# Performance work log

Hardware: AMD Instinct MI355X
Metric: run time of the kernel (lower is better)

Reference implementation:

```python
import jax, jax.numpy as jnp
import numpy as np

B, S, D_IN, M, H, F, L, D_OUT = 4, 1024, 256, 1024, 16, 8, 2, 256
HD = M // H
EPS = 1e-5


def setup_inputs() -> dict:
    key = jax.random.key(0)
    ks = iter(jax.random.split(key, 40))
    w = lambda *s: 0.02 * jax.random.normal(next(ks), s, dtype=jnp.float32)
    inp = {
        "x": jax.random.normal(next(ks), (B, S, D_IN), dtype=jnp.float32),
        # phase embedding params
        "Wemb": w(D_IN, M), "bemb": w(M),
        "Wamp": w(M, F), "bamp": w(F),
        "freqs": jnp.logspace(-1, 2, F, dtype=jnp.float32),
        "phase_off": w(F),
        # per-layer attention params, stacked on leading L axis
        "Wq": w(L, M, M), "bq": w(L, M),
        "Wk": w(L, M, M), "bk": w(L, M),
        "Wv": w(L, M, M), "bv": w(L, M),
        "Wo": w(L, M, M), "bo": w(L, M),
        "pbias": w(L, H, F),
        "ln_g": jnp.ones((L, M), dtype=jnp.float32),
        "ln_b": jnp.zeros((L, M), dtype=jnp.float32),
        # output projection MLP
        "W1": w(M, M // 2), "b1": w(M // 2),
        "W2": w(M // 2, D_OUT), "b2": w(D_OUT),
    }
    return inp


def _forward(x, Wemb, bemb, Wamp, bamp, freqs, phase_off,
             Wq, bq, Wk, bk, Wv, bv, Wo, bo, pbias, ln_g, ln_b,
             W1, b1, W2, b2):
    Bsz, Seq, _ = x.shape
    # --- TemporalPhaseEmbedding ---
    m = x @ Wemb + bemb                                   # [B,S,M]
    tc = jnp.arange(Seq, dtype=x.dtype) / Seq * (2.0 * jnp.pi)  # [S]
    amp = jax.nn.softmax(m @ Wamp + bamp, axis=-1)        # [B,S,F]
    pc = tc[:, None] * freqs[None, :] + phase_off         # [S,F] (batch-identical)
    # |m[...,None] * amp * e^{i*pc}| averaged over F == |m| * mean_F(amp)
    pf = jnp.abs(m) * jnp.mean(amp, axis=-1, keepdims=True)  # [B,S,M]
    # phase-coherence, batch-independent since pc is shared across batch
    coh = jnp.cos(pc[:, None, :] - pc[None, :, :])        # [S,S,F]
    scale = 1.0 / jnp.sqrt(jnp.asarray(HD, dtype=x.dtype))
    for l in range(L):
        res = pf
        Q = (pf @ Wq[l] + bq[l]).reshape(Bsz, Seq, H, HD)
        K = (pf @ Wk[l] + bk[l]).reshape(Bsz, Seq, H, HD)
        V = (pf @ Wv[l] + bv[l]).reshape(Bsz, Seq, H, HD)
        bias = jnp.einsum('stf,hf->hst', coh, pbias[l])   # [H,S,S]
        scores = jnp.einsum('bshd,bthd->bhst', Q, K) * scale + bias[None]
        w_attn = jax.nn.softmax(scores, axis=-1)
        att = jnp.einsum('bhst,bthd->bshd', w_attn, V).reshape(Bsz, Seq, M)
        att = att @ Wo[l] + bo[l]
        y = att + res
        mu = jnp.mean(y, axis=-1, keepdims=True)
        var = jnp.var(y, axis=-1, keepdims=True)
        pf = (y - mu) / jnp.sqrt(var + EPS) * ln_g[l] + ln_b[l]
    hdn = jax.nn.relu(pf @ W1 + b1)
    return hdn @ W2 + b2                                  # [B,S,D_OUT]


def reference(x, Wemb, bemb, Wamp, bamp, freqs, phase_off,
              Wq, bq, Wk, bk, Wv, bv, Wo, bo, pbias, ln_g, ln_b,
              W1, b1, W2, b2):
    return _forward(x, Wemb, bemb, Wamp, bamp, freqs, phase_off,
                    Wq, bq, Wk, bk, Wv, bv, Wo, bo, pbias, ln_g, ln_b,
                    W1, b1, W2, b2)
```

## Files before the change

### kernel.cpp

```cpp
#include <hip/hip_runtime.h>
#include <cmath>

#define B_    4
#define S_    1024
#define DIN_  256
#define M_    1024
#define H_    16
#define F_    8
#define L_    2
#define DOUT_ 256
#define NT_   4096

typedef unsigned short u16;
typedef unsigned int   u32;
typedef __bf16 bf16x8 __attribute__((ext_vector_type(8)));
typedef __bf16 bf16x4v __attribute__((ext_vector_type(4)));
typedef float  f32x4  __attribute__((ext_vector_type(4)));

#define LOG2E 1.4426950408889634f
#define QSCALE (0.125f * LOG2E)

__device__ __forceinline__ u16 f2b(float f) {
    u32 u = __builtin_bit_cast(u32, f);
    u += 0x7fffu + ((u >> 16) & 1u);
    return (u16)(u >> 16);
}
__device__ __forceinline__ float b2f(u32 h) {
    return __builtin_bit_cast(float, h << 16);
}
__device__ __forceinline__ void gload_lds16(const void* g, void* l) {
    __builtin_amdgcn_global_load_lds(
        (const __attribute__((address_space(1))) u32*)g,
        (__attribute__((address_space(3))) u32*)l, 16, 0, 0);
}

__device__ __forceinline__ void tileT(float (*t)[33], const float* src,
                                      u16* dst, int K, int N, int n0, int k0,
                                      int tid)
{
    const int r = tid >> 3, c4 = (tid & 7) << 2;
    float4 v = *(const float4*)(src + (size_t)(k0 + r) * N + n0 + c4);
    t[r][c4 + 0] = v.x; t[r][c4 + 1] = v.y; t[r][c4 + 2] = v.z; t[r][c4 + 3] = v.w;
    __syncthreads();
    ushort4 o = make_ushort4(f2b(t[c4 + 0][r]), f2b(t[c4 + 1][r]),
                             f2b(t[c4 + 2][r]), f2b(t[c4 + 3][r]));
    *(ushort4*)(dst + (size_t)(n0 + r) * K + k0 + c4) = o;
}

__global__ __launch_bounds__(256) void prep_k(
    const float* __restrict__ x, const float* __restrict__ Wemb,
    const float* __restrict__ Wq, const float* __restrict__ Wk,
    const float* __restrict__ Wv, const float* __restrict__ Wo,
    const float* __restrict__ W1, const float* __restrict__ W2,
    const float* __restrict__ freqs, const float* __restrict__ poff,
    const float* __restrict__ pb, const float* __restrict__ bq,
    const float* __restrict__ bk, const float* __restrict__ bv,
    u16* __restrict__ xb, u16* __restrict__ WembT, u16* __restrict__ WqkvT,
    u16* __restrict__ WoT, u16* __restrict__ W1T, u16* __restrict__ W2T,
    u16* __restrict__ qcs, u16* __restrict__ csb, float* __restrict__ bqkv)
{
    __shared__ float t[32][33];
    const int bid = blockIdx.x, tid = threadIdx.x;

    if (bid < 1024) {
        int i = (bid * 256 + tid) * 4;
        float4 v = *(const float4*)(x + i);
        *(ushort4*)(xb + i) = make_ushort4(f2b(v.x), f2b(v.y), f2b(v.z), f2b(v.w));
    } else if (bid < 7168) {
        int id = bid - 1024;
        int z = id >> 10, rem = id & 1023;
        int n0 = (rem & 31) << 5, k0 = (rem >> 5) << 5;
        int l = z / 3, which = z - l * 3;
        const float* src = (which == 0 ? Wq : which == 1 ? Wk : Wv) + (size_t)l * M_ * M_;
        u16* d = WqkvT + (size_t)l * 3072 * 1024 + (size_t)which * 1024 * 1024;
        tileT(t, src, d, 1024, 1024, n0, k0, tid);
    } else if (bid < 9216) {
        int id = bid - 7168;
        int z = id >> 10, rem = id & 1023;
        int n0 = (rem & 31) << 5, k0 = (rem >> 5) << 5;
        tileT(t, Wo + (size_t)z * M_ * M_, WoT + (size_t)z * M_ * M_,
              1024, 1024, n0, k0, tid);
    } else if (bid < 9472) {
        int id = bid - 9216;
        int n0 = (id & 31) << 5, k0 = (id >> 5) << 5;
        tileT(t, Wemb, WembT, 256, 1024, n0, k0, tid);
    } else if (bid < 9984) {
        int id = bid - 9472;
        int n0 = (id & 15) << 5, k0 = (id >> 4) << 5;
        tileT(t, W1, W1T, 1024, 512, n0, k0, tid);
    } else if (bid < 10112) {
        int id = bid - 9984;
        int n0 = (id & 7) << 5, k0 = (id >> 3) << 5;
        tileT(t, W2, W2T, 512, 256, n0, k0, tid);
    } else if (bid < 12224) {
        const int QN = L_ * H_ * S_ * 16;
        int idx = (bid - 10112) * 256 + tid;
        if (idx < QN) {
            int f2 = idx & 15, f = f2 & 7;
            int s = (idx >> 4) & 1023;
            int lh = idx >> 14;
            float pc = ((float)s * (6.283185307179586f / 1024.f)) * freqs[f] + poff[f];
            float v = (f2 < 8) ? cosf(pc) : sinf(pc);
            qcs[idx] = f2b(pb[lh * 8 + f] * v * LOG2E);
        } else {
            int i2 = idx - QN;
            int f2 = i2 & 15, f = f2 & 7;
            int s = i2 >> 4;
            float pc = ((float)s * (6.283185307179586f / 1024.f)) * freqs[f] + poff[f];
            csb[i2] = f2b((f2 < 8) ? cosf(pc) : sinf(pc));
        }
    } else {
        int idx = (bid - 12224) * 256 + tid;
        int l = idx >= 3072;
        int j = idx - l * 3072;
        float v = (j < 1024) ? bq[l * 1024 + j]
                : (j < 2048) ? bk[l * 1024 + j - 1024]
                             : bv[l * 1024 + j - 2048];
        bqkv[idx] = v;
    }
}

template<int EPI, int OUTBF, int BM>
__global__ __launch_bounds__(256, 2) void mgemm_k(
    const u16* __restrict__ A, const u16* __restrict__ Wt,
    const float* __restrict__ bias, void* __restrict__ Cout,
    u16* __restrict__ vt, int N, int K)
{
    constexpr int MR = BM / 32;
    __shared__ __attribute__((aligned(16))) u16 As[BM * 64];
    __shared__ __attribute__((aligned(16))) u16 Bs[128 * 64];
    const int tid = threadIdx.x;
    const int lane = tid & 63;
    const int bn = blockIdx.x, bm = blockIdx.y;
    const int wid = tid >> 6, wr = wid >> 1, wc = wid & 1;

    f32x4 acc[MR][4];
#pragma unroll
    for (int m = 0; m < MR; ++m)
#pragma unroll
        for (int n = 0; n < 4; ++n) {
            f32x4 z = {0.f, 0.f, 0.f, 0.f};
            acc[m][n] = z;
        }

    const int r = lane & 15, g = lane >> 4;
    const int nk = K >> 6;

    for (int kt = 0; kt < nk; ++kt) {
        const int k0 = kt << 6;
        __syncthreads();
#pragma unroll
        for (int i = 0; i < (BM >> 5); ++i) {
            int slot = i * 256 + tid;
            int row = slot >> 3;
            int kg = (slot & 7) ^ (row & 7);
            gload_lds16(A + (size_t)(bm * BM + row) * K + k0 + kg * 8,
                        As + (size_t)(slot & ~63) * 8);
        }
#pragma unroll
        for (int i = 0; i < 4; ++i) {
            int slot = i * 256 + tid;
            int row = slot >> 3;
            int kg = (slot & 7) ^ (row & 7);
            gload_lds16(Wt + (size_t)(bn * 128 + row) * K + k0 + kg * 8,
                        Bs + (size_t)(slot & ~63) * 8);
        }
        __syncthreads();

#pragma unroll
        for (int ks = 0; ks < 2; ++ks) {
            bf16x8 af[MR], bfr[4];
#pragma unroll
            for (int m = 0; m < MR; ++m) {
                int row = wr * (BM >> 1) + m * 16 + r;
                int kg = (ks * 4 + g) ^ (row & 7);
                af[m] = *(const bf16x8*)(As + row * 64 + kg * 8);
            }
#pragma unroll
            for (int n = 0; n < 4; ++n) {
                int row = wc * 64 + n * 16 + r;
                int kg = (ks * 4 + g) ^ (row & 7);
                bfr[n] = *(const bf16x8*)(Bs + row * 64 + kg * 8);
            }
#pragma unroll
            for (int m = 0; m < MR; ++m)
#pragma unroll
                for (int n = 0; n < 4; ++n)
                    acc[m][n] = __builtin_amdgcn_mfma_f32_16x16x32_bf16(
                        af[m], bfr[n], acc[m][n], 0, 0, 0);
        }
    }

#pragma unroll
    for (int n = 0; n < 4; ++n) {
        const int gcol = bn * 128 + wc * 64 + n * 16 + r;
        const float bb = bias[gcol];
#pragma unroll
        for (int m = 0; m < MR; ++m) {
            const int grow0 = bm * BM + wr * (BM >> 1) + m * 16 + g * 4;
            if (EPI == 5 && gcol >= 2048) {
                int d = gcol - 2048;
                int bh = (grow0 >> 10) * 16 + (d >> 6);
                u16 pk[4];
#pragma unroll
                for (int q = 0; q < 4; ++q) pk[q] = f2b(acc[m][n][q] + bb);
                uint2 pv;
                pv.x = (u32)pk[0] | ((u32)pk[1] << 16);
                pv.y = (u32)pk[2] | ((u32)pk[3] << 16);
                *(uint2*)(vt + ((size_t)bh * 64 + (d & 63)) * 1024 + (grow0 & 1023)) = pv;
            } else {
#pragma unroll
                for (int q = 0; q < 4; ++q) {
                    float c = acc[m][n][q] + bb;
                    if (EPI == 1) c = fabsf(c) * 0.125f;
                    if (EPI == 2) c = fmaxf(c, 0.f);
                    if (EPI == 5) c = (gcol < 1024) ? c * QSCALE : c;
                    if (EPI == 6)
                        c += b2f(vt[(size_t)(grow0 + q) * N + gcol]);
                    if (OUTBF)
                        ((u16*)Cout)[(size_t)(grow0 + q) * N + gcol] = f2b(c);
                    else
                        ((float*)Cout)[(size_t)(grow0 + q) * N + gcol] = c;
                }
            }
        }
    }
}

__global__ __launch_bounds__(256) void fattn_k(
    const u16* __restrict__ QKV, const u16* __restrict__ Vtg,
    const u16* __restrict__ csb, const u16* __restrict__ qcs,
    u16* __restrict__ Og)
{
    __shared__ __attribute__((aligned(16))) u16 Ks3[3][64 * 64];
    __shared__ __attribute__((aligned(16))) u16 Vt3[3][64 * 64];
    __shared__ __attribute__((aligned(16))) u16 Ext[3][64 * 16];
    __shared__ __attribute__((aligned(16))) u16 Pl[4][32 * 68];
    const int tid = threadIdx.x, lane = tid & 63, w = tid >> 6;
    const int c = lane & 15, g = lane >> 4;
    const int Lid = blockIdx.x;
    const int slot = Lid >> 3;
    const int grp = (Lid & 7) * 8 + (slot >> 3);
    const int qi = slot & 7;
    const int b = grp >> 4, h = grp & 15, bh = grp;
    const int s0 = qi * 128;

    const uint4 zz = {0u, 0u, 0u, 0u};
    const bf16x8 zfrag = __builtin_bit_cast(bf16x8, zz);

    bf16x8 aq[2][3];
#pragma unroll
    for (int m = 0; m < 2; ++m) {
        int sl = s0 + w * 32 + m * 16 + c;
        size_t tok = (size_t)b * 1024 + sl;
        aq[m][0] = *(const bf16x8*)(QKV + tok * 3072 + h * 64 + g * 8);
        aq[m][1] = *(const bf16x8*)(QKV + tok * 3072 + h * 64 + 32 + g * 8);
        aq[m][2] = (g < 2) ? *(const bf16x8*)(qcs + ((size_t)h * 1024 + sl) * 16 + g * 8)
                           : zfrag;
    }
    __builtin_amdgcn_sched_barrier(0);

    f32x4 oacc[2][4];
#pragma unroll
    for (int m = 0; m < 2; ++m)
#pragma unroll
        for (int n = 0; n < 4; ++n) {
            f32x4 z = {0.f, 0.f, 0.f, 0.f};
            oacc[m][n] = z;
        }
    float lsum[2] = {0.f, 0.f};

    auto STAGE = [&](int buf, int t0) {
#pragma unroll
        for (int i = 0; i < 2; ++i) {
            int sl2 = i * 256 + tid;
            int row = sl2 >> 3, gi = sl2 & 7;
            int kg = (gi ^ (row & 7)) * 8;
            gload_lds16(QKV + (size_t)(b * 1024 + t0 + row) * 3072 + 1024 + h * 64 + kg,
                        &Ks3[buf][(size_t)(sl2 & ~63) * 8]);
            gload_lds16(Vtg + (size_t)(bh * 64 + row) * 1024 + t0 + kg,
                        &Vt3[buf][(size_t)(sl2 & ~63) * 8]);
        }
        if (tid < 128) {
            int r2 = tid >> 1, g2 = tid & 1;
            gload_lds16(csb + (size_t)(t0 + r2) * 16 + g2 * 8,
                        &Ext[buf][(size_t)(tid & ~63) * 8]);
        }
    };

    STAGE(0, 0);
    STAGE(1, 64);
    __builtin_amdgcn_sched_barrier(0);

    int cur = 0;
    for (int it = 0; it < 16; ++it) {
        if (it < 14) {
            int nb = cur + 2; if (nb >= 3) nb -= 3;
            STAGE(nb, (it + 2) << 6);
            if (w < 2) asm volatile("s_waitcnt vmcnt(10)" ::: "memory");
            else       asm volatile("s_waitcnt vmcnt(8)" ::: "memory");
        } else if (it == 14) {
            if (w < 2) asm volatile("s_waitcnt vmcnt(5)" ::: "memory");
            else       asm volatile("s_waitcnt vmcnt(4)" ::: "memory");
        } else {
            asm volatile("s_waitcnt vmcnt(0)" ::: "memory");
        }
        __builtin_amdgcn_sched_barrier(0);
        __builtin_amdgcn_s_barrier();
        __builtin_amdgcn_sched_barrier(0);

        const u16* ksb = &Ks3[cur][0];
        const u16* vtb = &Vt3[cur][0];
        const u16* exb = &Ext[cur][0];

        f32x4 sacc[2][4];
#pragma unroll
        for (int m = 0; m < 2; ++m)
#pragma unroll
            for (int n = 0; n < 4; ++n) {
                f32x4 z = {0.f, 0.f, 0.f, 0.f};
                sacc[m][n] = z;
            }
        __builtin_amdgcn_s_setprio(1);
#pragma unroll
        for (int ks = 0; ks < 3; ++ks) {
            bf16x8 bk[4];
#pragma unroll
            for (int n = 0; n < 4; ++n) {
                int tr = n * 16 + c;
                if (ks < 2) {
                    int kg = (ks * 4 + g) ^ (tr & 7);
                    bk[n] = *(const bf16x8*)(ksb + tr * 64 + kg * 8);
                } else {
                    bk[n] = (g < 2) ? *(const bf16x8*)(exb + tr * 16 + g * 8) : zfrag;
                }
            }
#pragma unroll
            for (int n = 0; n < 4; ++n)
#pragma unroll
                for (int m = 0; m < 2; ++m)
                    sacc[m][n] = __builtin_amdgcn_mfma_f32_16x16x32_bf16(
                        bk[n], aq[m][ks], sacc[m][n], 0, 0, 0);
        }
        __builtin_amdgcn_s_setprio(0);

#pragma unroll
        for (int m = 0; m < 2; ++m)
#pragma unroll
            for (int n = 0; n < 4; ++n) {
                float p0 = __builtin_amdgcn_exp2f(sacc[m][n][0]);
                float p1 = __builtin_amdgcn_exp2f(sacc[m][n][1]);
                float p2 = __builtin_amdgcn_exp2f(sacc[m][n][2]);
                float p3 = __builtin_amdgcn_exp2f(sacc[m][n][3]);
                lsum[m] += (p0 + p1) + (p2 + p3);
                bf16x4v pk;
                pk[0] = (__bf16)p0; pk[1] = (__bf16)p1;
                pk[2] = (__bf16)p2; pk[3] = (__bf16)p3;
                *(bf16x4v*)(&Pl[w][(m * 16 + c) * 68 + n * 16 + g * 4]) = pk;
            }

        __builtin_amdgcn_s_setprio(1);
#pragma unroll
        for (int ks2 = 0; ks2 < 2; ++ks2) {
            bf16x8 pa[2];
#pragma unroll
            for (int m = 0; m < 2; ++m)
                pa[m] = *(const bf16x8*)(&Pl[w][(m * 16 + c) * 68 + ks2 * 32 + g * 8]);
#pragma unroll
            for (int n = 0; n < 4; ++n) {
                int dr = n * 16 + c;
                int kg = (ks2 * 4 + g) ^ (dr & 7);
                bf16x8 vf = *(const bf16x8*)(vtb + dr * 64 + kg * 8);
#pragma unroll
                for (int m = 0; m < 2; ++m)
                    oacc[m][n] = __builtin_amdgcn_mfma_f32_16x16x32_bf16(
                        pa[m], vf, oacc[m][n], 0, 0, 0);
            }
        }
        __builtin_amdgcn_s_setprio(0);

        __builtin_amdgcn_sched_barrier(0);
        __builtin_amdgcn_s_barrier();
        __builtin_amdgcn_sched_barrier(0);
        cur = (cur == 2) ? 0 : cur + 1;
    }

#pragma unroll
    for (int m = 0; m < 2; ++m) {
        float lt = lsum[m] + __shfl_xor(lsum[m], 16);
        lt += __shfl_xor(lt, 32);
        float inv[4];
#pragma unroll
        for (int q = 0; q < 4; ++q)
            inv[q] = 1.f / __shfl(lt, g * 4 + q);
#pragma unroll
        for (int n = 0; n < 4; ++n)
#pragma unroll
            for (int q = 0; q < 4; ++q) {
                size_t tok = (size_t)b * 1024 + s0 + w * 32 + m * 16 + g * 4 + q;
                Og[tok * 1024 + h * 64 + n * 16 + c] = f2b(oacc[m][n][q] * inv[q]);
            }
    }
}

__global__ __launch_bounds__(256) void ln_k(
    const u16* __restrict__ Yr, u16* __restrict__ Pf,
    const float* __restrict__ g, const float* __restrict__ bt)
{
    const int rw = blockIdx.x;
    const int tid = threadIdx.x;
    const u16* yp = Yr + (size_t)rw * M_ + tid * 4;
    u16* pp = Pf + (size_t)rw * M_ + tid * 4;
    ushort4 yv = *(const ushort4*)yp;
    float a[4];
    a[0] = b2f(yv.x); a[1] = b2f(yv.y);
    a[2] = b2f(yv.z); a[3] = b2f(yv.w);
    float s = a[0] + a[1] + a[2] + a[3];
    float q = a[0] * a[0] + a[1] * a[1] + a[2] * a[2] + a[3] * a[3];
#pragma unroll
    for (int o = 1; o < 64; o <<= 1) {
        s += __shfl_xor(s, o);
        q += __shfl_xor(q, o);
    }
    __shared__ float ss[4], qq[4];
    if ((tid & 63) == 0) { ss[tid >> 6] = s; qq[tid >> 6] = q; }
    __syncthreads();
    s = ss[0] + ss[1] + ss[2] + ss[3];
    q = qq[0] + qq[1] + qq[2] + qq[3];
    float mu = s * (1.0f / 1024.0f);
    float var = q * (1.0f / 1024.0f) - mu * mu;
    float inv = rsqrtf(var + 1e-5f);
    float4 gv = *(const float4*)(g + (tid << 2));
    float4 bv = *(const float4*)(bt + (tid << 2));
    *(ushort4*)pp = make_ushort4(
        f2b((a[0] - mu) * inv * gv.x + bv.x),
        f2b((a[1] - mu) * inv * gv.y + bv.y),
        f2b((a[2] - mu) * inv * gv.z + bv.z),
        f2b((a[3] - mu) * inv * gv.w + bv.w));
}

extern "C" void kernel_launch(void* const* d_in, const int* in_sizes, int n_in,
                              void* d_out, int out_size, void* d_ws, size_t ws_size,
                              hipStream_t stream)
{
    const float* x     = (const float*)d_in[0];
    const float* Wemb  = (const float*)d_in[1];
    const float* bemb  = (const float*)d_in[2];
    const float* freqs = (const float*)d_in[5];
    const float* poff  = (const float*)d_in[6];
    const float* Wq    = (const float*)d_in[7];
    const float* bq    = (const float*)d_in[8];
    const float* Wk    = (const float*)d_in[9];
    const float* bk    = (const float*)d_in[10];
    const float* Wv    = (const float*)d_in[11];
    const float* bv    = (const float*)d_in[12];
    const float* Wo    = (const float*)d_in[13];
    const float* bo    = (const float*)d_in[14];
    const float* pbias = (const float*)d_in[15];
    const float* lng   = (const float*)d_in[16];
    const float* lnb   = (const float*)d_in[17];
    const float* W1    = (const float*)d_in[18];
    const float* b1    = (const float*)d_in[19];
    const float* W2    = (const float*)d_in[20];
    const float* b2    = (const float*)d_in[21];
    float* out = (float*)d_out;

    char* ws = (char*)d_ws;
    const size_t MB = 1 << 20;
    u16* pf    = (u16*)(ws);
    u16* QKV   = (u16*)(ws + 8 * MB);
    u16* Ab    = (u16*)(ws + 32 * MB);
    u16* Vtg   = (u16*)(ws + 40 * MB);
    u16* WqkvT = (u16*)(ws + 48 * MB);
    u16* WoT   = (u16*)(ws + 60 * MB);
    u16* WembT = (u16*)(ws + 64 * MB);
    u16* W1T   = (u16*)(ws + 64 * MB + 512 * 1024);
    u16* W2T   = (u16*)(ws + 65 * MB + 512 * 1024);
    u16* xb    = (u16*)(ws + 66 * MB);
    u16* qcs   = (u16*)(ws + 68 * MB);
    u16* csb   = (u16*)(ws + 69 * MB);
    float* bqkv = (float*)(ws + 69 * MB + 64 * 1024);

    dim3 blk(256);
    prep_k<<<12248, blk, 0, stream>>>(x, Wemb, Wq, Wk, Wv, Wo, W1, W2,
                                      freqs, poff, pbias, bq, bk, bv,
                                      xb, WembT, WqkvT, WoT, W1T, W2T,
                                      qcs, csb, bqkv);

    mgemm_k<1, 1, 64><<<dim3(8, 64), blk, 0, stream>>>(xb, WembT, bemb, pf, nullptr, 1024, 256);

    for (int l = 0; l < L_; ++l) {
        mgemm_k<5, 1, 128><<<dim3(24, 32), blk, 0, stream>>>(
            pf, WqkvT + (size_t)l * 3072 * 1024, bqkv + l * 3072, QKV, Vtg, 3072, 1024);
        fattn_k<<<dim3(512), blk, 0, stream>>>(
            QKV, Vtg, csb, qcs + (size_t)l * H_ * S_ * 16, Ab);
        mgemm_k<6, 1, 64><<<dim3(8, 64), blk, 0, stream>>>(
            Ab, WoT + (size_t)l * M_ * M_, bo + l * M_, QKV , pf, 1024, 1024);
        ln_k<<<dim3(NT_), blk, 0, stream>>>(QKV, pf, lng + l * M_, lnb + l * M_);
    }

    mgemm_k<2, 1, 64><<<dim3(4, 64), blk, 0, stream>>>(pf, W1T, b1, Ab, nullptr, 512, 1024);
    mgemm_k<0, 0, 64><<<dim3(2, 64), blk, 0, stream>>>(Ab, W2T, b2, out, nullptr, 256, 512);
}
```

Measured before the change: 237.5 us.

## Add 256x256-tile triple-buffered QKV GEMM kernel and compact sincos prep

Replaces the generic 128x128-tile QKV projection GEMM with a dedicated 512-thread kernel using 256x256 tiles, a 3-stage LDS ring filled by direct global-to-LDS loads with explicit vmcnt waits, XOR-swizzled LDS layout, and MFMA priority boosting. It aims to increase operand reuse and overlap memory with compute, at the cost of only 192 blocks (less than one wave across the CUs) and heavy register use. The prep kernel also computes each sin/cos once with __sincosf and writes all 32 layer-head scaled copies from it, which shrinks the prep grid and cuts redundant transcendental work. __sincosf is a lower-precision intrinsic than cosf/sinf.

```diff
diff --git a/kernel.cpp b/kernel.cpp
--- a/kernel.cpp
+++ b/kernel.cpp
@@ -92,31 +92,139 @@
         int id = bid - 9984;
         int n0 = (id & 7) << 5, k0 = (id >> 3) << 5;
         tileT(t, W2, W2T, 512, 256, n0, k0, tid);
-    } else if (bid < 12224) {
-        const int QN = L_ * H_ * S_ * 16;
+    } else if (bid < 10144) {
         int idx = (bid - 10112) * 256 + tid;
-        if (idx < QN) {
-            int f2 = idx & 15, f = f2 & 7;
-            int s = (idx >> 4) & 1023;
-            int lh = idx >> 14;
-            float pc = ((float)s * (6.283185307179586f / 1024.f)) * freqs[f] + poff[f];
-            float v = (f2 < 8) ? cosf(pc) : sinf(pc);
-            qcs[idx] = f2b(pb[lh * 8 + f] * v * LOG2E);
-        } else {
-            int i2 = idx - QN;
-            int f2 = i2 & 15, f = f2 & 7;
-            int s = i2 >> 4;
-            float pc = ((float)s * (6.283185307179586f / 1024.f)) * freqs[f] + poff[f];
-            csb[i2] = f2b((f2 < 8) ? cosf(pc) : sinf(pc));
+        int s = idx >> 3, f = idx & 7;
+        float pc = ((float)s * (6.283185307179586f / 1024.f)) * freqs[f] + poff[f];
+        float sn, cs;
+        __sincosf(pc, &sn, &cs);
+        csb[s * 16 + f] = f2b(cs);
+        csb[s * 16 + f + 8] = f2b(sn);
+#pragma unroll
+        for (int lh = 0; lh < 32; ++lh) {
+            float p = pb[lh * 8 + f] * LOG2E;
+            qcs[lh * 16384 + s * 16 + f] = f2b(p * cs);
+            qcs[lh * 16384 + s * 16 + f + 8] = f2b(p * sn);
         }
     } else {
-        int idx = (bid - 12224) * 256 + tid;
+        int idx = (bid - 10144) * 256 + tid;
         int l = idx >= 3072;
         int j = idx - l * 3072;
         float v = (j < 1024) ? bq[l * 1024 + j]
                 : (j < 2048) ? bk[l * 1024 + j - 1024]
                              : bv[l * 1024 + j - 2048];
         bqkv[idx] = v;
+    }
+}
+
+__global__ __launch_bounds__(512, 2) void qkv256_k(
+    const u16* __restrict__ A, const u16* __restrict__ Wt,
+    const float* __restrict__ bias, u16* __restrict__ Cout,
+    u16* __restrict__ vt)
+{
+    __shared__ __attribute__((aligned(16))) u16 As[3 * 256 * 32];
+    __shared__ __attribute__((aligned(16))) u16 Bs[3 * 256 * 32];
+    const int tid = threadIdx.x, lane = tid & 63;
+    const int wid = tid >> 6, wr = wid >> 2, wc = wid & 3;
+    const int r = lane & 15, g = lane >> 4;
+    const int bn = blockIdx.x % 12, bm = blockIdx.x / 12;
+    const int K = 1024;
+
+    f32x4 acc[8][4];
+#pragma unroll
+    for (int mf = 0; mf < 8; ++mf)
+#pragma unroll
+        for (int nf = 0; nf < 4; ++nf) {
+            f32x4 z = {0.f, 0.f, 0.f, 0.f};
+            acc[mf][nf] = z;
+        }
+
+    auto STAGE = [&](int slot, int kt) {
+        u16* As0 = As + slot * (256 * 32);
+        u16* Bs0 = Bs + slot * (256 * 32);
+#pragma unroll
+        for (int i = 0; i < 2; ++i) {
+            int s = i * 512 + tid;
+            int row = s >> 2, gi = s & 3;
+            int kg = gi ^ ((row >> 2) & 3);
+            gload_lds16(A + (size_t)(bm * 256 + row) * K + kt * 32 + kg * 8,
+                        As0 + (size_t)(s & ~63) * 8);
+            gload_lds16(Wt + (size_t)(bn * 256 + row) * K + kt * 32 + kg * 8,
+                        Bs0 + (size_t)(s & ~63) * 8);
+        }
+    };
+
+    STAGE(0, 0);
+    STAGE(1, 1);
+    __builtin_amdgcn_sched_barrier(0);
+
+    int slot = 0;
+    for (int t = 0; t < 32; ++t) {
+        if (t < 30) {
+            int nb = slot + 2; if (nb >= 3) nb -= 3;
+            STAGE(nb, t + 2);
+            asm volatile("s_waitcnt vmcnt(8)" ::: "memory");
+        } else if (t == 30) {
+            asm volatile("s_waitcnt vmcnt(4)" ::: "memory");
+        } else {
+            asm volatile("s_waitcnt vmcnt(0)" ::: "memory");
+        }
+        __builtin_amdgcn_sched_barrier(0);
+        __builtin_amdgcn_s_barrier();
+        __builtin_amdgcn_sched_barrier(0);
+
+        const u16* As0 = As + slot * (256 * 32);
+        const u16* Bs0 = Bs + slot * (256 * 32);
+        bf16x8 af[8], bfr[4];
+        const int kg = (g ^ ((r >> 2) & 3)) * 8;
+#pragma unroll
+        for (int mf = 0; mf < 8; ++mf)
+            af[mf] = *(const bf16x8*)(As0 + (wr * 128 + mf * 16 + r) * 32 + kg);
+#pragma unroll
+        for (int nf = 0; nf < 4; ++nf)
+            bfr[nf] = *(const bf16x8*)(Bs0 + (wc * 64 + nf * 16 + r) * 32 + kg);
+
+        __builtin_amdgcn_s_setprio(1);
+#pragma unroll
+        for (int mf = 0; mf < 8; ++mf)
+#pragma unroll
+            for (int nf = 0; nf < 4; ++nf)
+                acc[mf][nf] = __builtin_amdgcn_mfma_f32_16x16x32_bf16(
+                    af[mf], bfr[nf], acc[mf][nf], 0, 0, 0);
+        __builtin_amdgcn_s_setprio(0);
+
+        __builtin_amdgcn_sched_barrier(0);
+        __builtin_amdgcn_s_barrier();
+        __builtin_amdgcn_sched_barrier(0);
+        slot = (slot == 2) ? 0 : slot + 1;
+    }
+
+#pragma unroll
+    for (int nf = 0; nf < 4; ++nf) {
+        const int gcol = bn * 256 + wc * 64 + nf * 16 + r;
+        const float bb = bias[gcol];
+#pragma unroll
+        for (int mf = 0; mf < 8; ++mf) {
+            const int grow0 = bm * 256 + wr * 128 + mf * 16 + g * 4;
+            if (gcol >= 2048) {
+                int d = gcol - 2048;
+                int bh = (grow0 >> 10) * 16 + (d >> 6);
+                u16 pk[4];
+#pragma unroll
+                for (int q = 0; q < 4; ++q) pk[q] = f2b(acc[mf][nf][q] + bb);
+                uint2 pv;
+                pv.x = (u32)pk[0] | ((u32)pk[1] << 16);
+                pv.y = (u32)pk[2] | ((u32)pk[3] << 16);
+                *(uint2*)(vt + ((size_t)bh * 64 + (d & 63)) * 1024 + (grow0 & 1023)) = pv;
+            } else {
+                const float sc = (gcol < 1024) ? QSCALE : 1.f;
+#pragma unroll
+                for (int q = 0; q < 4; ++q) {
+                    float c = (acc[mf][nf][q] + bb) * sc;
+                    Cout[(size_t)(grow0 + q) * 3072 + gcol] = f2b(c);
+                }
+            }
+        }
     }
 }
 
@@ -198,30 +306,17 @@
 #pragma unroll
         for (int m = 0; m < MR; ++m) {
             const int grow0 = bm * BM + wr * (BM >> 1) + m * 16 + g * 4;
-            if (EPI == 5 && gcol >= 2048) {
-                int d = gcol - 2048;
-                int bh = (grow0 >> 10) * 16 + (d >> 6);
-                u16 pk[4];
-#pragma unroll
-                for (int q = 0; q < 4; ++q) pk[q] = f2b(acc[m][n][q] + bb);
-                uint2 pv;
-                pv.x = (u32)pk[0] | ((u32)pk[1] << 16);
-                pv.y = (u32)pk[2] | ((u32)pk[3] << 16);
-                *(uint2*)(vt + ((size_t)bh * 64 + (d & 63)) * 1024 + (grow0 & 1023)) = pv;
-            } else {
-#pragma unroll
-                for (int q = 0; q < 4; ++q) {
-                    float c = acc[m][n][q] + bb;
-                    if (EPI == 1) c = fabsf(c) * 0.125f;
-                    if (EPI == 2) c = fmaxf(c, 0.f);
-                    if (EPI == 5) c = (gcol < 1024) ? c * QSCALE : c;
-                    if (EPI == 6)
-                        c += b2f(vt[(size_t)(grow0 + q) * N + gcol]);
-                    if (OUTBF)
-                        ((u16*)Cout)[(size_t)(grow0 + q) * N + gcol] = f2b(c);
-                    else
-                        ((float*)Cout)[(size_t)(grow0 + q) * N + gcol] = c;
-                }
+#pragma unroll
+            for (int q = 0; q < 4; ++q) {
+                float c = acc[m][n][q] + bb;
+                if (EPI == 1) c = fabsf(c) * 0.125f;
+                if (EPI == 2) c = fmaxf(c, 0.f);
+                if (EPI == 6)
+                    c += b2f(vt[(size_t)(grow0 + q) * N + gcol]);
+                if (OUTBF)
+                    ((u16*)Cout)[(size_t)(grow0 + q) * N + gcol] = f2b(c);
+                else
+                    ((float*)Cout)[(size_t)(grow0 + q) * N + gcol] = c;
             }
         }
     }
@@ -482,7 +577,7 @@
     float* bqkv = (float*)(ws + 69 * MB + 64 * 1024);
 
     dim3 blk(256);
-    prep_k<<<12248, blk, 0, stream>>>(x, Wemb, Wq, Wk, Wv, Wo, W1, W2,
+    prep_k<<<10168, blk, 0, stream>>>(x, Wemb, Wq, Wk, Wv, Wo, W1, W2,
                                       freqs, poff, pbias, bq, bk, bv,
                                       xb, WembT, WqkvT, WoT, W1T, W2T,
                                       qcs, csb, bqkv);
@@ -490,8 +585,8 @@
     mgemm_k<1, 1, 64><<<dim3(8, 64), blk, 0, stream>>>(xb, WembT, bemb, pf, nullptr, 1024, 256);
 
     for (int l = 0; l < L_; ++l) {
-        mgemm_k<5, 1, 128><<<dim3(24, 32), blk, 0, stream>>>(
-            pf, WqkvT + (size_t)l * 3072 * 1024, bqkv + l * 3072, QKV, Vtg, 3072, 1024);
+        qkv256_k<<<dim3(192), dim3(512), 0, stream>>>(
+            pf, WqkvT + (size_t)l * 3072 * 1024, bqkv + l * 3072, QKV, Vtg);
         fattn_k<<<dim3(512), blk, 0, stream>>>(
             QKV, Vtg, csb, qcs + (size_t)l * H_ * S_ * 16, Ab);
         mgemm_k<6, 1, 64><<<dim3(8, 64), blk, 0, stream>>>(
```

After: 259.3 us. 9.2% more time.
